# Optimization experiments

Measured on AMD Instinct MI355X. Metric: run time of the kernel, lower is better.

## Reference

```python
import jax, jax.numpy as jnp
import numpy as np

B, P, F = 512, 512, 1024
EPS = 1e-8


def setup_inputs() -> dict:
    key = jax.random.key(0)
    k1, k2 = jax.random.split(key)
    x = jax.random.normal(k1, (B, F), dtype=jnp.float32)
    # kaiming_normal_(fan_in, relu): std = sqrt(2 / fan_in)
    weight = jax.random.normal(k2, (P, F), dtype=jnp.float32) * np.float32(np.sqrt(2.0 / F))
    bias = jnp.zeros((P,), dtype=jnp.float32)
    alpha = jnp.ones((), dtype=jnp.float32)
    beta = jnp.ones((), dtype=jnp.float32)
    return {"x": x, "weight": weight, "bias": bias, "alpha": alpha, "beta": beta}


def reference(x, weight, bias, alpha, beta):
    # x: (B, F), weight: (P, F)
    x_sig = jax.nn.sigmoid(x)[:, None, :]        # (B, 1, F)
    w_sig = jax.nn.sigmoid(weight)[None, :, :]   # (1, P, F)
    intersection = jnp.minimum(x_sig, w_sig).sum(axis=-1)          # (B, P)
    x_diff = jnp.maximum(x_sig - w_sig, 0.0).sum(axis=-1)          # (B, P)
    w_diff = jnp.maximum(w_sig - x_sig, 0.0).sum(axis=-1)          # (B, P)
    denom = intersection + alpha * x_diff + beta * w_diff + EPS
    return intersection / denom + bias
```

## Files before the change

### kernel.cpp

```cpp
#include <hip/hip_runtime.h>

#define FDIM 1024
#define FD4 256
#define BDIM 512
#define PDIM 512

__device__ __forceinline__ unsigned sad8(unsigned a, unsigned b, unsigned c) {
  return __builtin_amdgcn_sad_u8(a, b, c);
}

__device__ __forceinline__ unsigned quant4(float4 v) {
  float s0 = 1.f / (1.f + __expf(-v.x));
  float s1 = 1.f / (1.f + __expf(-v.y));
  float s2 = 1.f / (1.f + __expf(-v.z));
  float s3 = 1.f / (1.f + __expf(-v.w));
  unsigned q0 = (unsigned)(s0 * 255.f + 0.5f);
  unsigned q1 = (unsigned)(s1 * 255.f + 0.5f);
  unsigned q2 = (unsigned)(s2 * 255.f + 0.5f);
  unsigned q3 = (unsigned)(s3 * 255.f + 0.5f);
  return q0 | (q1 << 8) | (q2 << 16) | (q3 << 24);
}

__global__ __launch_bounds__(256) void quant_kernel(
    const float* __restrict__ x, const float* __restrict__ w,
    unsigned* __restrict__ xqT, unsigned* __restrict__ wq) {
  __shared__ unsigned lt[64 * 33];
  const int tid = threadIdx.x;
  if (blockIdx.x < PDIM) {
    const int row = blockIdx.x;
    float4 v = ((const float4*)(w + (size_t)row * FDIM))[tid];
    wq[row * FD4 + tid] = quant4(v);
  } else {
    const int t = blockIdx.x - PDIM;
    const int r0 = (t & 7) * 64;
    const int d0 = (t >> 3) * 32;
#pragma unroll
    for (int k = 0; k < 8; ++k) {
      const int flat = tid + 256 * k;
      const int row = flat >> 5;
      const int c = flat & 31;
      float4 v = ((const float4*)x)[(r0 + row) * FD4 + d0 + c];
      lt[row * 33 + c] = quant4(v);
    }
    __syncthreads();
#pragma unroll
    for (int k = 0; k < 8; ++k) {
      const int flat = tid + 256 * k;
      const int dc = flat >> 6;
      const int b = flat & 63;
      xqT[(d0 + dc) * BDIM + r0 + b] = lt[b * 33 + dc];
    }
  }
}

__global__ __launch_bounds__(256) void tversky_pair(
    const unsigned* __restrict__ xqT, const unsigned* __restrict__ wq,
    const float* __restrict__ bias, const float* __restrict__ alphap,
    const float* __restrict__ betap, float* __restrict__ out) {
  const int tid = threadIdx.x;
  const int lane = tid & 63;
  const int wv = __builtin_amdgcn_readfirstlane(tid >> 6);
  const int r = blockIdx.y * 64 + lane;
  const int c0 = blockIdx.x * 8;

  __shared__ unsigned part[4][8][64];
  __shared__ unsigned sxp[4][64];
  __shared__ unsigned swsum[8];
  if (tid < 8) swsum[tid] = 0;
  __syncthreads();

  unsigned xv[64];
#pragma unroll
  for (int k = 0; k < 64; ++k) xv[k] = xqT[(wv * 64 + k) * BDIM + r];

  unsigned sx = 0;
#pragma unroll
  for (int k = 0; k < 64; ++k) sx = sad8(xv[k], 0u, sx);
  sxp[wv][lane] = sx;

  {
    const int wrow = tid >> 5;
    const int seg = tid & 31;
    const unsigned* wp = wq + (c0 + wrow) * FD4 + seg * 8;
    unsigned s = 0;
#pragma unroll
    for (int j = 0; j < 8; ++j) s = sad8(wp[j], 0u, s);
    atomicAdd(&swsum[wrow], s);
  }

  for (int pp = 0; pp < 8; ++pp) {
    const unsigned* wp = wq + (c0 + pp) * FD4 + wv * 64;
    unsigned a0 = 0, a1 = 0, a2 = 0, a3 = 0;
#pragma unroll
    for (int j = 0; j < 16; ++j) {
      a0 = sad8(xv[4 * j + 0], wp[4 * j + 0], a0);
      a1 = sad8(xv[4 * j + 1], wp[4 * j + 1], a1);
      a2 = sad8(xv[4 * j + 2], wp[4 * j + 2], a2);
      a3 = sad8(xv[4 * j + 3], wp[4 * j + 3], a3);
    }
    part[wv][pp][lane] = a0 + a1 + a2 + a3;
  }
  __syncthreads();

  const float alpha = alphap[0];
  const float beta = betap[0];
#pragma unroll
  for (int id = tid; id < 512; id += 256) {
    const int row = id >> 3;
    const int pp = id & 7;
    const unsigned D = part[0][pp][row] + part[1][pp][row] +
                       part[2][pp][row] + part[3][pp][row];
    const unsigned Sxi = sxp[0][row] + sxp[1][row] + sxp[2][row] + sxp[3][row];
    const unsigned Swi = swsum[pp];
    const int b = blockIdx.y * 64 + row;
    const int p = c0 + pp;
    const float fSx = (float)Sxi;
    const float fSw = (float)Swi;
    const float I = 0.5f * (fSx + fSw - (float)D);
    const float denom = I + alpha * (fSx - I) + beta * (fSw - I) + 255.0f * 1e-8f;
    out[b * PDIM + p] = I / denom + bias[p];
  }
}

extern "C" void kernel_launch(void* const* d_in, const int* in_sizes, int n_in,
                              void* d_out, int out_size, void* d_ws, size_t ws_size,
                              hipStream_t stream) {
  const float* x = (const float*)d_in[0];
  const float* w = (const float*)d_in[1];
  const float* bias = (const float*)d_in[2];
  const float* alpha = (const float*)d_in[3];
  const float* beta = (const float*)d_in[4];
  float* out = (float*)d_out;

  unsigned char* ws = (unsigned char*)d_ws;
  unsigned* xqT = (unsigned*)ws;
  unsigned* wq = (unsigned*)(ws + 512 * 1024);

  quant_kernel<<<dim3(PDIM + 64), dim3(256), 0, stream>>>(x, w, xqT, wq);
  tversky_pair<<<dim3(PDIM / 8, BDIM / 64), dim3(256), 0, stream>>>(
      xqT, wq, bias, alpha, beta, out);
}
```

Baseline: 71.68 us.

## Fuse sigmoid quantization into pair kernel using shared-memory staging

Removes the separate quantization kernel and workspace. Each block now quantizes its own 64 x rows (transposed into LDS) and 8 weight rows into LDS, then computes SAD-based Tversky scores from shared memory. This eliminates one launch and the global write/read of quantized data. The cost is redundant sigmoid/quantization of x across column blocks and high LDS use that limits occupancy. Partial sums are also narrowed to 16-bit in LDS.

```diff
diff --git a/kernel.cpp b/kernel.cpp
--- a/kernel.cpp
+++ b/kernel.cpp
@@ -21,84 +21,76 @@
   return q0 | (q1 << 8) | (q2 << 16) | (q3 << 24);
 }
 
-__global__ __launch_bounds__(256) void quant_kernel(
+__global__ __launch_bounds__(256) void tversky_fused(
     const float* __restrict__ x, const float* __restrict__ w,
-    unsigned* __restrict__ xqT, unsigned* __restrict__ wq) {
-  __shared__ unsigned lt[64 * 33];
-  const int tid = threadIdx.x;
-  if (blockIdx.x < PDIM) {
-    const int row = blockIdx.x;
-    float4 v = ((const float4*)(w + (size_t)row * FDIM))[tid];
-    wq[row * FD4 + tid] = quant4(v);
-  } else {
-    const int t = blockIdx.x - PDIM;
-    const int r0 = (t & 7) * 64;
-    const int d0 = (t >> 3) * 32;
-#pragma unroll
-    for (int k = 0; k < 8; ++k) {
-      const int flat = tid + 256 * k;
-      const int row = flat >> 5;
-      const int c = flat & 31;
-      float4 v = ((const float4*)x)[(r0 + row) * FD4 + d0 + c];
-      lt[row * 33 + c] = quant4(v);
-    }
-    __syncthreads();
-#pragma unroll
-    for (int k = 0; k < 8; ++k) {
-      const int flat = tid + 256 * k;
-      const int dc = flat >> 6;
-      const int b = flat & 63;
-      xqT[(d0 + dc) * BDIM + r0 + b] = lt[b * 33 + dc];
-    }
-  }
-}
-
-__global__ __launch_bounds__(256) void tversky_pair(
-    const unsigned* __restrict__ xqT, const unsigned* __restrict__ wq,
     const float* __restrict__ bias, const float* __restrict__ alphap,
     const float* __restrict__ betap, float* __restrict__ out) {
+  __shared__ unsigned xT[FD4][65];
+  __shared__ __align__(16) unsigned wqs[8][FD4];
+  __shared__ unsigned short part[4][8][64];
+  __shared__ unsigned short sxp[4][64];
+  __shared__ unsigned swsum[8];
+
   const int tid = threadIdx.x;
   const int lane = tid & 63;
   const int wv = __builtin_amdgcn_readfirstlane(tid >> 6);
-  const int r = blockIdx.y * 64 + lane;
+  const int r0 = blockIdx.y * 64;
   const int c0 = blockIdx.x * 8;
 
-  __shared__ unsigned part[4][8][64];
-  __shared__ unsigned sxp[4][64];
-  __shared__ unsigned swsum[8];
   if (tid < 8) swsum[tid] = 0;
+
+  const float4* __restrict__ xf4 = (const float4*)x;
+  const float4* __restrict__ wf4 = (const float4*)w;
+
+#pragma unroll
+  for (int j = 0; j < 8; ++j) {
+    wqs[j][tid] = quant4(wf4[(size_t)(c0 + j) * FD4 + tid]);
+  }
+
+#pragma unroll 2
+  for (int ii = 0; ii < 8; ++ii) {
+    float4 v[8];
+#pragma unroll
+    for (int j = 0; j < 8; ++j)
+      v[j] = xf4[(size_t)(r0 + ii * 8 + j) * FD4 + tid];
+#pragma unroll
+    for (int j = 0; j < 8; ++j) xT[tid][ii * 8 + j] = quant4(v[j]);
+  }
   __syncthreads();
 
   unsigned xv[64];
 #pragma unroll
-  for (int k = 0; k < 64; ++k) xv[k] = xqT[(wv * 64 + k) * BDIM + r];
+  for (int k = 0; k < 64; ++k) xv[k] = xT[wv * 64 + k][lane];
 
   unsigned sx = 0;
 #pragma unroll
   for (int k = 0; k < 64; ++k) sx = sad8(xv[k], 0u, sx);
-  sxp[wv][lane] = sx;
+  sxp[wv][lane] = (unsigned short)sx;
 
   {
     const int wrow = tid >> 5;
     const int seg = tid & 31;
-    const unsigned* wp = wq + (c0 + wrow) * FD4 + seg * 8;
+    const uint4* wp = (const uint4*)&wqs[wrow][seg * 8];
+    const uint4 q0 = wp[0], q1 = wp[1];
     unsigned s = 0;
-#pragma unroll
-    for (int j = 0; j < 8; ++j) s = sad8(wp[j], 0u, s);
+    s = sad8(q0.x, 0u, s); s = sad8(q0.y, 0u, s);
+    s = sad8(q0.z, 0u, s); s = sad8(q0.w, 0u, s);
+    s = sad8(q1.x, 0u, s); s = sad8(q1.y, 0u, s);
+    s = sad8(q1.z, 0u, s); s = sad8(q1.w, 0u, s);
     atomicAdd(&swsum[wrow], s);
   }
 
   for (int pp = 0; pp < 8; ++pp) {
-    const unsigned* wp = wq + (c0 + pp) * FD4 + wv * 64;
     unsigned a0 = 0, a1 = 0, a2 = 0, a3 = 0;
 #pragma unroll
     for (int j = 0; j < 16; ++j) {
-      a0 = sad8(xv[4 * j + 0], wp[4 * j + 0], a0);
-      a1 = sad8(xv[4 * j + 1], wp[4 * j + 1], a1);
-      a2 = sad8(xv[4 * j + 2], wp[4 * j + 2], a2);
-      a3 = sad8(xv[4 * j + 3], wp[4 * j + 3], a3);
+      const uint4 q = *(const uint4*)&wqs[pp][wv * 64 + 4 * j];
+      a0 = sad8(xv[4 * j + 0], q.x, a0);
+      a1 = sad8(xv[4 * j + 1], q.y, a1);
+      a2 = sad8(xv[4 * j + 2], q.z, a2);
+      a3 = sad8(xv[4 * j + 3], q.w, a3);
     }
-    part[wv][pp][lane] = a0 + a1 + a2 + a3;
+    part[wv][pp][lane] = (unsigned short)(a0 + a1 + a2 + a3);
   }
   __syncthreads();
 
@@ -108,17 +100,16 @@
   for (int id = tid; id < 512; id += 256) {
     const int row = id >> 3;
     const int pp = id & 7;
-    const unsigned D = part[0][pp][row] + part[1][pp][row] +
+    const unsigned D = (unsigned)part[0][pp][row] + part[1][pp][row] +
                        part[2][pp][row] + part[3][pp][row];
-    const unsigned Sxi = sxp[0][row] + sxp[1][row] + sxp[2][row] + sxp[3][row];
+    const unsigned Sxi = (unsigned)sxp[0][row] + sxp[1][row] +
+                         sxp[2][row] + sxp[3][row];
     const unsigned Swi = swsum[pp];
-    const int b = blockIdx.y * 64 + row;
-    const int p = c0 + pp;
     const float fSx = (float)Sxi;
     const float fSw = (float)Swi;
     const float I = 0.5f * (fSx + fSw - (float)D);
     const float denom = I + alpha * (fSx - I) + beta * (fSw - I) + 255.0f * 1e-8f;
-    out[b * PDIM + p] = I / denom + bias[p];
+    out[(r0 + row) * PDIM + (c0 + pp)] = I / denom + bias[c0 + pp];
   }
 }
 
@@ -131,12 +122,8 @@
   const float* alpha = (const float*)d_in[3];
   const float* beta = (const float*)d_in[4];
   float* out = (float*)d_out;
+  (void)in_sizes; (void)n_in; (void)d_ws; (void)ws_size;
 
-  unsigned char* ws = (unsigned char*)d_ws;
-  unsigned* xqT = (unsigned*)ws;
-  unsigned* wq = (unsigned*)(ws + 512 * 1024);
-
-  quant_kernel<<<dim3(PDIM + 64), dim3(256), 0, stream>>>(x, w, xqT, wq);
-  tversky_pair<<<dim3(PDIM / 8, BDIM / 64), dim3(256), 0, stream>>>(
-      xqT, wq, bias, alpha, beta, out);
+  tversky_fused<<<dim3(PDIM / 8, BDIM / 64), dim3(256), 0, stream>>>(
+      x, w, bias, alpha, beta, out);
 }
```

Result: slower. 87.32 us (+21.8%).

## Fuse quantize and pair kernels into one cooperative kernel with grid sync

Applied to the files above, without the earlier changes.

Merges the quantization/transposition kernel and the pairwise SAD kernel into a single cooperative launch of 512 blocks. Each block first quantizes one weight row and a 64x4 tile of x, then a grid-wide sync separates that phase from the pairwise compute. This removes a kernel launch and the gap between the two kernels, at the cost of a grid barrier and cooperative-launch overhead. Each block's transpose tile shrinks, so xqT stores become narrower.

```diff
diff --git a/kernel.cpp b/kernel.cpp
--- a/kernel.cpp
+++ b/kernel.cpp
@@ -1,4 +1,7 @@
 #include <hip/hip_runtime.h>
+#include <hip/hip_cooperative_groups.h>
+
+namespace cg = cooperative_groups;
 
 #define FDIM 1024
 #define FD4 256
@@ -21,51 +24,49 @@
   return q0 | (q1 << 8) | (q2 << 16) | (q3 << 24);
 }
 
-__global__ __launch_bounds__(256) void quant_kernel(
+__global__ __launch_bounds__(256) void tversky_coop(
     const float* __restrict__ x, const float* __restrict__ w,
+    const float* __restrict__ bias, const float* __restrict__ alphap,
+    const float* __restrict__ betap, float* __restrict__ out,
     unsigned* __restrict__ xqT, unsigned* __restrict__ wq) {
-  __shared__ unsigned lt[64 * 33];
-  const int tid = threadIdx.x;
-  if (blockIdx.x < PDIM) {
-    const int row = blockIdx.x;
-    float4 v = ((const float4*)(w + (size_t)row * FDIM))[tid];
-    wq[row * FD4 + tid] = quant4(v);
-  } else {
-    const int t = blockIdx.x - PDIM;
-    const int r0 = (t & 7) * 64;
-    const int d0 = (t >> 3) * 32;
-#pragma unroll
-    for (int k = 0; k < 8; ++k) {
-      const int flat = tid + 256 * k;
-      const int row = flat >> 5;
-      const int c = flat & 31;
-      float4 v = ((const float4*)x)[(r0 + row) * FD4 + d0 + c];
-      lt[row * 33 + c] = quant4(v);
-    }
-    __syncthreads();
-#pragma unroll
-    for (int k = 0; k < 8; ++k) {
-      const int flat = tid + 256 * k;
-      const int dc = flat >> 6;
-      const int b = flat & 63;
-      xqT[(d0 + dc) * BDIM + r0 + b] = lt[b * 33 + dc];
-    }
-  }
-}
-
-__global__ __launch_bounds__(256) void tversky_pair(
-    const unsigned* __restrict__ xqT, const unsigned* __restrict__ wq,
-    const float* __restrict__ bias, const float* __restrict__ alphap,
-    const float* __restrict__ betap, float* __restrict__ out) {
-  const int tid = threadIdx.x;
-  const int lane = tid & 63;
-  const int wv = __builtin_amdgcn_readfirstlane(tid >> 6);
-  const int r = blockIdx.y * 64 + lane;
-  const int c0 = blockIdx.x * 8;
-
+  __shared__ unsigned lt[64][5];
   __shared__ unsigned part[4][8][64];
   __shared__ unsigned sxp[4][64];
   __shared__ unsigned swsum[8];
+
+  const int tid = threadIdx.x;
+  const int blk = blockIdx.x;
+
+  {
+    float4 v = ((const float4*)(w + (size_t)blk * FDIM))[tid];
+    wq[blk * FD4 + tid] = quant4(v);
+  }
+
+  {
+    const int rt = blk >> 6;
+    const int ct = blk & 63;
+    const int r0 = rt * 64;
+    const int d0 = ct * 4;
+    const int row = tid >> 2;
+    const int c = tid & 3;
+    float4 v = ((const float4*)x)[(size_t)(r0 + row) * FD4 + d0 + c];
+    lt[row][c] = quant4(v);
+    __syncthreads();
+    const int c2 = tid >> 6;
+    const int b = tid & 63;
+    xqT[(size_t)(d0 + c2) * BDIM + r0 + b] = lt[b][c2];
+  }
+
+  __threadfence();
+  cg::this_grid().sync();
+
+  const int lane = tid & 63;
+  const int wv = __builtin_amdgcn_readfirstlane(tid >> 6);
+  const int bx = blk & 63;
+  const int by = blk >> 6;
+  const int r = by * 64 + lane;
+  const int c0 = bx * 8;
+
   if (tid < 8) swsum[tid] = 0;
   __syncthreads();
 
@@ -112,7 +113,7 @@
                        part[2][pp][row] + part[3][pp][row];
     const unsigned Sxi = sxp[0][row] + sxp[1][row] + sxp[2][row] + sxp[3][row];
     const unsigned Swi = swsum[pp];
-    const int b = blockIdx.y * 64 + row;
+    const int b = by * 64 + row;
     const int p = c0 + pp;
     const float fSx = (float)Sxi;
     const float fSw = (float)Swi;
@@ -135,8 +136,10 @@
   unsigned char* ws = (unsigned char*)d_ws;
   unsigned* xqT = (unsigned*)ws;
   unsigned* wq = (unsigned*)(ws + 512 * 1024);
+  (void)in_sizes; (void)n_in; (void)ws_size;
 
-  quant_kernel<<<dim3(PDIM + 64), dim3(256), 0, stream>>>(x, w, xqT, wq);
-  tversky_pair<<<dim3(PDIM / 8, BDIM / 64), dim3(256), 0, stream>>>(
-      xqT, wq, bias, alpha, beta, out);
+  void* args[] = {(void*)&x, (void*)&w, (void*)&bias, (void*)&alpha,
+                  (void*)&beta, (void*)&out, (void*)&xqT, (void*)&wq};
+  hipLaunchCooperativeKernel((void*)tversky_coop, dim3(512), dim3(256), args,
+                             0, stream);
 }
```

After: 192.3 us. +168.3%, slower.
